# Performance work log

Measured on AMD Instinct MI355X. Metric: run time of the kernel, lower is better.

## Reference

```python
import jax, jax.numpy as jnp
import numpy as np

N, E, DIM, H, EDIM = 50000, 800000, 128, 4, 16
C = DIM // H  # per-head channels = 32

def _ln(x, g, b, eps=1e-5):
    mu = jnp.mean(x, -1, keepdims=True)
    var = jnp.mean((x - mu) ** 2, -1, keepdims=True)
    return (x - mu) * jax.lax.rsqrt(var + eps) * g + b

def setup_inputs() -> dict:
    key = jax.random.key(0)
    ks = jax.random.split(key, 16)
    s = lambda d: 1.0 / np.sqrt(d)
    inp = {
        'x': jax.random.normal(ks[0], (N, DIM), jnp.float32),
        'edge_index_s': jax.random.randint(ks[1], (2, E), 0, N, jnp.int64),
        'edge_attr_s': jax.random.normal(ks[2], (E, EDIM), jnp.float32),
        'Wq': jax.random.normal(ks[3], (DIM, DIM), jnp.float32) * s(DIM),
        'bq': jnp.zeros((DIM,), jnp.float32),
        'Wk': jax.random.normal(ks[4], (DIM, DIM), jnp.float32) * s(DIM),
        'bk': jnp.zeros((DIM,), jnp.float32),
        'Wv': jax.random.normal(ks[5], (DIM, DIM), jnp.float32) * s(DIM),
        'bv': jnp.zeros((DIM,), jnp.float32),
        'We': jax.random.normal(ks[6], (EDIM, DIM), jnp.float32) * s(EDIM),
        'be': jnp.zeros((DIM,), jnp.float32),
        'Ws': jax.random.normal(ks[7], (DIM, DIM), jnp.float32) * s(DIM),
        'bs': jnp.zeros((DIM,), jnp.float32),
        'Wbeta': jax.random.normal(ks[8], (3 * DIM, 1), jnp.float32) * s(3 * DIM),
        'g1': jnp.ones((DIM,), jnp.float32),
        'b1': jnp.zeros((DIM,), jnp.float32),
        'Wf1': jax.random.normal(ks[9], (DIM, 4 * DIM), jnp.float32) * s(DIM),
        'bf1': jnp.zeros((4 * DIM,), jnp.float32),
        'Wf2': jax.random.normal(ks[10], (4 * DIM, DIM), jnp.float32) * s(4 * DIM),
        'bf2': jnp.zeros((DIM,), jnp.float32),
        'g2': jnp.ones((DIM,), jnp.float32),
        'b2': jnp.zeros((DIM,), jnp.float32),
    }
    return inp

def reference(x, edge_index_s, edge_attr_s, Wq, bq, Wk, bk, Wv, bv, We, be,
              Ws, bs, Wbeta, g1, b1, Wf1, bf1, Wf2, bf2, g2, b2):
    src, dst = edge_index_s[0], edge_index_s[1]
    # project + reshape to [N, H, C]
    q = (x @ Wq + bq).reshape(N, H, C)
    k = (x @ Wk + bk).reshape(N, H, C)
    v = (x @ Wv + bv).reshape(N, H, C)
    e = (edge_attr_s @ We + be).reshape(E, H, C)
    # gather along edges (irregular access)
    kj = k[src] + e  # [E, H, C]
    vj = v[src] + e
    alpha = jnp.einsum('ehc,ehc->eh', q[dst], kj) / jnp.sqrt(jnp.float32(C))
    # segment softmax over incoming edges of each dst node
    m = jax.ops.segment_max(alpha, dst, num_segments=N)  # [N, H]
    a = jnp.exp(alpha - m[dst])
    denom = jax.ops.segment_sum(a, dst, num_segments=N)
    a = a / (denom[dst] + 1e-16)
    out = jax.ops.segment_sum(a[:, :, None] * vj, dst, num_segments=N)  # [N, H, C]
    out = out.reshape(N, DIM)
    # beta-gated skip (TransformerConv beta=True)
    xr = x @ Ws + bs
    beta = jax.nn.sigmoid(jnp.concatenate([out, xr, out - xr], -1) @ Wbeta)  # [N, 1]
    xs = beta * xr + (1.0 - beta) * out
    # residual + LN + FFN + LN
    h = _ln(x + xs, g1, b1)
    ff = jax.nn.relu(h @ Wf1 + bf1) @ Wf2 + bf2
    return _ln(h + ff, g2, b2)
```

## Files before the change

kernel.cpp:

```cpp
#include <hip/hip_runtime.h>
#include <hip/hip_bf16.h>

#define NN 50000
#define EE 800000
#define DIMM 128

typedef __attribute__((ext_vector_type(8))) short bf16x8;
typedef __attribute__((ext_vector_type(8))) unsigned short us8;
typedef __attribute__((ext_vector_type(4))) float f32x4;

static __device__ __forceinline__ unsigned short f2bf(float f) {
    unsigned int u = __float_as_uint(f);
    unsigned int r = (u + 0x7fffu + ((u >> 16) & 1u)) >> 16;
    return (unsigned short)r;
}
static __device__ __forceinline__ float bf2f(unsigned short s) {
    return __uint_as_float(((unsigned int)s) << 16);
}

__global__ __launch_bounds__(256) void pack_w(
    const float* __restrict__ Wq, const float* __restrict__ Wk,
    const float* __restrict__ Wv, const float* __restrict__ Ws,
    const float* __restrict__ bq, const float* __restrict__ bk,
    const float* __restrict__ bv, const float* __restrict__ bs,
    const float* __restrict__ Wf1, const float* __restrict__ Wf2,
    unsigned short* __restrict__ wqkvsT, unsigned short* __restrict__ wf1T,
    unsigned short* __restrict__ wf2T, float* __restrict__ biasq)
{
    int i = blockIdx.x * 256 + threadIdx.x;
    if (i < 65536) {
        int n = i >> 7, k = i & 127;
        int sel = n >> 7, col = n & 127;
        const float* W = sel == 0 ? Wq : sel == 1 ? Wk : sel == 2 ? Wv : Ws;
        wqkvsT[i] = f2bf(W[k * 128 + col]);
    } else if (i < 131072) {
        int j = i - 65536; int n = j >> 7, k = j & 127;
        wf1T[j] = f2bf(Wf1[k * 512 + n]);
    } else if (i < 196608) {
        int j = i - 131072; int n = j >> 9, k = j & 511;
        wf2T[j] = f2bf(Wf2[k * 128 + n]);
    } else if (i < 197120) {
        int j = i - 196608; int sel = j >> 7;
        const float* bp = sel == 0 ? bq : sel == 1 ? bk : sel == 2 ? bv : bs;
        biasq[j] = bp[j & 127];
    }
}

template<bool A_BF16, int EPI>
__global__ __launch_bounds__(256) void gemm_k(
    const void* __restrict__ Ap, const unsigned short* __restrict__ Bt,
    const float* __restrict__ bias, void* __restrict__ Cp,
    float* __restrict__ qb, unsigned short* __restrict__ kvb, float* __restrict__ xrb,
    int M, int Nn, int K)
{
    __shared__ unsigned short As[128][72];
    __shared__ unsigned short Bs[64][72];
    int tid = threadIdx.x;
    int nb = Nn >> 6;
    int bm = blockIdx.x / nb, bn = blockIdx.x % nb;
    int w = tid >> 6, lane = tid & 63;
    int wm = w >> 1, wn = w & 1;
    int lr = lane & 15, quad = lane >> 4;

    f32x4 acc[4][2];
    #pragma unroll
    for (int i = 0; i < 4; i++)
        #pragma unroll
        for (int j = 0; j < 2; j++) { f32x4 z = {0.f, 0.f, 0.f, 0.f}; acc[i][j] = z; }

    for (int kc = 0; kc < K; kc += 64) {
        #pragma unroll
        for (int it = 0; it < 4; ++it) {
            int row = it * 32 + (tid >> 3);
            int k8 = (tid & 7) * 8;
            int rg = bm * 128 + row;
            us8 st = {0, 0, 0, 0, 0, 0, 0, 0};
            if (rg < M) {
                if constexpr (A_BF16) {
                    st = *(const us8*)((const unsigned short*)Ap + (size_t)rg * K + kc + k8);
                } else {
                    const float* src = (const float*)Ap + (size_t)rg * K + kc + k8;
                    float4 f0 = *(const float4*)src;
                    float4 f1 = *(const float4*)(src + 4);
                    st[0] = f2bf(f0.x); st[1] = f2bf(f0.y); st[2] = f2bf(f0.z); st[3] = f2bf(f0.w);
                    st[4] = f2bf(f1.x); st[5] = f2bf(f1.y); st[6] = f2bf(f1.z); st[7] = f2bf(f1.w);
                }
            }
            *(us8*)&As[row][k8] = st;
        }
        {
            int nrow = tid >> 2;
            int k16 = (tid & 3) * 16;
            const unsigned short* src = Bt + (size_t)(bn * 64 + nrow) * K + kc + k16;
            *(us8*)&Bs[nrow][k16]     = *(const us8*)src;
            *(us8*)&Bs[nrow][k16 + 8] = *(const us8*)(src + 8);
        }
        __syncthreads();
        #pragma unroll
        for (int kk = 0; kk < 2; ++kk) {
            bf16x8 af[4], bfr[2];
            #pragma unroll
            for (int mi = 0; mi < 4; mi++)
                af[mi] = *(const bf16x8*)&As[wm * 64 + mi * 16 + lr][kk * 32 + quad * 8];
            #pragma unroll
            for (int ni = 0; ni < 2; ni++)
                bfr[ni] = *(const bf16x8*)&Bs[wn * 32 + ni * 16 + lr][kk * 32 + quad * 8];
            #pragma unroll
            for (int mi = 0; mi < 4; mi++)
                #pragma unroll
                for (int ni = 0; ni < 2; ni++)
                    acc[mi][ni] = __builtin_amdgcn_mfma_f32_16x16x32_bf16(af[mi], bfr[ni], acc[mi][ni], 0, 0, 0);
        }
        __syncthreads();
    }
    #pragma unroll
    for (int mi = 0; mi < 4; mi++) {
        #pragma unroll
        for (int ni = 0; ni < 2; ni++) {
            int cg = bn * 64 + wn * 32 + ni * 16 + lr;
            float bv = bias[cg];
            #pragma unroll
            for (int r = 0; r < 4; r++) {
                int rg = bm * 128 + wm * 64 + mi * 16 + quad * 4 + r;
                if (rg < M) {
                    float val = acc[mi][ni][r] + bv;
                    if constexpr (EPI == 0) {
                        ((float*)Cp)[(size_t)rg * Nn + cg] = val;
                    } else if constexpr (EPI == 1) {
                        val = fmaxf(val, 0.f);
                        ((unsigned short*)Cp)[(size_t)rg * Nn + cg] = f2bf(val);
                    } else {
                        int sel = cg >> 7, c = cg & 127;
                        if (sel == 0)      qb[(size_t)rg * 128 + c] = val;
                        else if (sel == 1) kvb[(size_t)rg * 256 + 2 * c] = f2bf(val);
                        else if (sel == 2) kvb[(size_t)rg * 256 + 2 * c + 1] = f2bf(val);
                        else               xrb[(size_t)rg * 128 + c] = val;
                    }
                }
            }
        }
    }
}

__global__ __launch_bounds__(256) void hist_k(const int* __restrict__ dst, int* __restrict__ deg) {
    int e = blockIdx.x * 256 + threadIdx.x;
    if (e < EE) atomicAdd(&deg[dst[e]], 1);
}

__global__ __launch_bounds__(256) void scan_phaseA(const int* __restrict__ deg, int* __restrict__ rs,
                                                   int* __restrict__ bsum) {
    __shared__ int sm[256];
    int tid = threadIdx.x;
    int i = blockIdx.x * 256 + tid;
    int v = (i < NN) ? deg[i] : 0;
    sm[tid] = v;
    __syncthreads();
    #pragma unroll
    for (int off = 1; off < 256; off <<= 1) {
        int t = 0;
        if (tid >= off) t = sm[tid - off];
        __syncthreads();
        if (tid >= off) sm[tid] += t;
        __syncthreads();
    }
    if (i < NN) rs[i] = sm[tid] - v;
    if (tid == 255) bsum[blockIdx.x] = sm[255];
}

__global__ __launch_bounds__(256) void scan_phaseB(int* __restrict__ bsum, int nb) {
    __shared__ int sm[256];
    int tid = threadIdx.x;
    int v = (tid < nb) ? bsum[tid] : 0;
    sm[tid] = v;
    __syncthreads();
    #pragma unroll
    for (int off = 1; off < 256; off <<= 1) {
        int t = 0;
        if (tid >= off) t = sm[tid - off];
        __syncthreads();
        if (tid >= off) sm[tid] += t;
        __syncthreads();
    }
    if (tid < nb) bsum[tid] = sm[tid] - v;
}

__global__ __launch_bounds__(256) void scan_phaseC(int* __restrict__ rs, const int* __restrict__ bsum) {
    int i = blockIdx.x * 256 + threadIdx.x;
    if (i < NN) rs[i] += bsum[blockIdx.x];
    if (i == 0) rs[NN] = EE;
}

__global__ __launch_bounds__(256) void scatter_k(
    const int* __restrict__ src, const int* __restrict__ dst,
    const float* __restrict__ eattr, const int* __restrict__ rs,
    int* __restrict__ cur, int* __restrict__ srcs_sorted,
    unsigned short* __restrict__ eas)
{
    int e = blockIdx.x * 256 + threadIdx.x;
    if (e < EE) {
        int d = dst[e];
        int p = atomicAdd(&cur[d], 1);
        int pos = rs[d] + p;
        srcs_sorted[pos] = src[e];
        const float* ap = eattr + (size_t)e * 16;
        float4 a0 = *(const float4*)ap;
        float4 a1 = *(const float4*)(ap + 4);
        float4 a2 = *(const float4*)(ap + 8);
        float4 a3 = *(const float4*)(ap + 12);
        us8 lo, hi;
        lo[0] = f2bf(a0.x); lo[1] = f2bf(a0.y); lo[2] = f2bf(a0.z); lo[3] = f2bf(a0.w);
        lo[4] = f2bf(a1.x); lo[5] = f2bf(a1.y); lo[6] = f2bf(a1.z); lo[7] = f2bf(a1.w);
        hi[0] = f2bf(a2.x); hi[1] = f2bf(a2.y); hi[2] = f2bf(a2.z); hi[3] = f2bf(a2.w);
        hi[4] = f2bf(a3.x); hi[5] = f2bf(a3.y); hi[6] = f2bf(a3.z); hi[7] = f2bf(a3.w);
        *(us8*)(eas + (size_t)pos * 16)     = lo;
        *(us8*)(eas + (size_t)pos * 16 + 8) = hi;
    }
}

__global__ __launch_bounds__(256, 3) void attn_kernel(
    const float* __restrict__ q, const unsigned int* __restrict__ kvb,
    const float* __restrict__ xr, const float* __restrict__ x,
    const unsigned short* __restrict__ eas, const int* __restrict__ srcs,
    const int* __restrict__ rs,
    const float* __restrict__ We, const float* __restrict__ be,
    const float* __restrict__ Wbeta,
    const float* __restrict__ gamma1, const float* __restrict__ beta1,
    float* __restrict__ hout, unsigned int* __restrict__ hbf)
{
    int wave = threadIdx.x >> 6;
    int lane = threadIdx.x & 63;
    int n = blockIdx.x * 4 + wave;
    if (n >= NN) return;
    int c0 = lane * 2, c1 = c0 + 1;
    int jlane = lane & 15;
    int hbase = lane & 48;

    float we0[16], we1[16];
    #pragma unroll
    for (int j = 0; j < 16; j++) { we0[j] = We[j * 128 + c0]; we1[j] = We[j * 128 + c1]; }
    float be0 = be[c0], be1 = be[c1];

    float2 q2 = *(const float2*)(q + (size_t)n * 128 + c0);
    q2.x *= 0.17677669529663687f;
    q2.y *= 0.17677669529663687f;

    float qbe = q2.x * be0 + q2.y * be1;
    qbe += __shfl_xor(qbe, 1); qbe += __shfl_xor(qbe, 2);
    qbe += __shfl_xor(qbe, 4); qbe += __shfl_xor(qbe, 8);
    float qwe = 0.f;
    #pragma unroll
    for (int j = 0; j < 16; j++) {
        float u = q2.x * we0[j] + q2.y * we1[j];
        u += __shfl_xor(u, 1); u += __shfl_xor(u, 2);
        u += __shfl_xor(u, 4); u += __shfl_xor(u, 8);
        if (jlane == j) qwe = u;
    }

    float l = 0.f, a0 = 0.f, a1 = 0.f, s = 0.f;
    int beg = rs[n], end = rs[n + 1];

    int sr_c[8]; unsigned short e_c[8];
    #pragma unroll
    for (int j = 0; j < 8; j++) {
        int idx = min(beg + j, EE - 1);
        sr_c[j] = srcs[idx];
        e_c[j] = eas[(size_t)idx * 16 + jlane];
    }
    for (int g = beg; g < end; g += 8) {
        uint2 kvp[8];
        #pragma unroll
        for (int j = 0; j < 8; j++)
            kvp[j] = *(const uint2*)(kvb + (size_t)sr_c[j] * 128 + (lane << 1));
        int gn = g + 8;
        int sr_n[8]; unsigned short e_n[8];
        #pragma unroll
        for (int j = 0; j < 8; j++) {
            int idx = min(gn + j, EE - 1);
            sr_n[j] = srcs[idx];
            e_n[j] = eas[(size_t)idx * 16 + jlane];
        }
        int cnt = end - g;
        #pragma unroll
        for (int j = 0; j < 8; j++) {
            if (j < cnt) {
                float ea = bf2f(e_c[j]);
                unsigned int kx = kvp[j].x, ky = kvp[j].y;
                float k0 = __uint_as_float(kx << 16);
                float v0 = __uint_as_float(kx & 0xffff0000u);
                float k1 = __uint_as_float(ky << 16);
                float v1 = __uint_as_float(ky & 0xffff0000u);
                float part = fmaf(q2.x, k0, fmaf(q2.y, k1, qwe * ea));
                part += __shfl_xor(part, 1);
                part += __shfl_xor(part, 2);
                part += __shfl_xor(part, 4);
                part += __shfl_xor(part, 8);
                float wgt = __expf(part + qbe);
                l += wgt;
                a0 = fmaf(wgt, v0, a0);
                a1 = fmaf(wgt, v1, a1);
                s = fmaf(wgt, ea, s);
            }
        }
        #pragma unroll
        for (int j = 0; j < 8; j++) { sr_c[j] = sr_n[j]; e_c[j] = e_n[j]; }
    }

    float eo0 = l * be0, eo1 = l * be1;
    #pragma unroll
    for (int j = 0; j < 16; j++) {
        float sj = __shfl(s, hbase + j);
        eo0 = fmaf(sj, we0[j], eo0);
        eo1 = fmaf(sj, we1[j], eo1);
    }
    a0 += eo0; a1 += eo1;

    float inv = l > 0.f ? 1.f / l : 0.f;
    float o0 = a0 * inv, o1 = a1 * inv;

    float wbo0 = Wbeta[c0],        wbo1 = Wbeta[c1];
    float wbx0 = Wbeta[128 + c0],  wbx1 = Wbeta[128 + c1];
    float wbd0 = Wbeta[256 + c0],  wbd1 = Wbeta[256 + c1];
    float2 xr2 = *(const float2*)(xr + (size_t)n * 128 + c0);
    float bl = o0 * wbo0 + o1 * wbo1 + xr2.x * wbx0 + xr2.y * wbx1
             + (o0 - xr2.x) * wbd0 + (o1 - xr2.y) * wbd1;
    #pragma unroll
    for (int off = 1; off < 64; off <<= 1) bl += __shfl_xor(bl, off);
    float beta = 1.f / (1.f + __expf(-bl));
    float xs0 = beta * xr2.x + (1.f - beta) * o0;
    float xs1 = beta * xr2.y + (1.f - beta) * o1;

    float2 xv = *(const float2*)(x + (size_t)n * 128 + c0);
    float t0 = xv.x + xs0, t1 = xv.y + xs1;
    float sm = t0 + t1;
    #pragma unroll
    for (int off = 1; off < 64; off <<= 1) sm += __shfl_xor(sm, off);
    float mu = sm * (1.f / 128.f);
    float d0 = t0 - mu, d1 = t1 - mu;
    float vv = d0 * d0 + d1 * d1;
    #pragma unroll
    for (int off = 1; off < 64; off <<= 1) vv += __shfl_xor(vv, off);
    float is = rsqrtf(vv * (1.f / 128.f) + 1e-5f);
    float h0 = d0 * is * gamma1[c0] + beta1[c0];
    float h1 = d1 * is * gamma1[c1] + beta1[c1];
    *(float2*)(hout + (size_t)n * 128 + c0) = make_float2(h0, h1);
    hbf[(size_t)n * 64 + lane] = (unsigned int)f2bf(h0) | ((unsigned int)f2bf(h1) << 16);
}

__global__ __launch_bounds__(256) void ln2_k(
    const float* __restrict__ h, const float* __restrict__ ff2,
    const float* __restrict__ gamma2, const float* __restrict__ beta2,
    float* __restrict__ out)
{
    int wave = threadIdx.x >> 6;
    int lane = threadIdx.x & 63;
    int n = blockIdx.x * 4 + wave;
    if (n >= NN) return;
    int c0 = lane * 2;
    float2 hv = *(const float2*)(h + (size_t)n * 128 + c0);
    float2 fv = *(const float2*)(ff2 + (size_t)n * 128 + c0);
    float t0 = hv.x + fv.x, t1 = hv.y + fv.y;
    float sm = t0 + t1;
    #pragma unroll
    for (int off = 1; off < 64; off <<= 1) sm += __shfl_xor(sm, off);
    float mu = sm * (1.f / 128.f);
    float d0 = t0 - mu, d1 = t1 - mu;
    float vv = d0 * d0 + d1 * d1;
    #pragma unroll
    for (int off = 1; off < 64; off <<= 1) vv += __shfl_xor(vv, off);
    float is = rsqrtf(vv * (1.f / 128.f) + 1e-5f);
    float o0 = d0 * is * gamma2[c0] + beta2[c0];
    float o1 = d1 * is * gamma2[c0 + 1] + beta2[c0 + 1];
    *(float2*)(out + (size_t)n * 128 + c0) = make_float2(o0, o1);
}

extern "C" void kernel_launch(void* const* d_in, const int* in_sizes, int n_in,
                              void* d_out, int out_size, void* d_ws, size_t ws_size,
                              hipStream_t stream) {
    const float* x      = (const float*)d_in[0];
    const int*   eindex = (const int*)d_in[1];
    const float* eattr  = (const float*)d_in[2];
    const float* Wq = (const float*)d_in[3];  const float* bq = (const float*)d_in[4];
    const float* Wk = (const float*)d_in[5];  const float* bk = (const float*)d_in[6];
    const float* Wv = (const float*)d_in[7];  const float* bv = (const float*)d_in[8];
    const float* We = (const float*)d_in[9];  const float* be = (const float*)d_in[10];
    const float* Ws = (const float*)d_in[11]; const float* bs = (const float*)d_in[12];
    const float* Wbeta = (const float*)d_in[13];
    const float* g1 = (const float*)d_in[14]; const float* b1 = (const float*)d_in[15];
    const float* Wf1 = (const float*)d_in[16]; const float* bf1 = (const float*)d_in[17];
    const float* Wf2 = (const float*)d_in[18]; const float* bf2 = (const float*)d_in[19];
    const float* g2 = (const float*)d_in[20]; const float* b2 = (const float*)d_in[21];

    char* ws = (char*)d_ws;
    size_t off = 0;
    #define ALLOC(ptr, type, bytes) type* ptr = (type*)(ws + off); off = (off + (size_t)(bytes) + 255) & ~(size_t)255;
    ALLOC(wqkvsT, unsigned short, 512 * 128 * 2)
    ALLOC(wf1T,   unsigned short, 512 * 128 * 2)
    ALLOC(wf2T,   unsigned short, 128 * 512 * 2)
    ALLOC(biasq,  float,          512 * 4)
    ALLOC(qb,     float,          (size_t)NN * 128 * 4)
    ALLOC(kvb,    unsigned short, (size_t)NN * 256 * 2)
    ALLOC(xrb,    float,          (size_t)NN * 128 * 4)
    ALLOC(h,      float,          (size_t)NN * 128 * 4)
    ALLOC(hbf,    unsigned int,   (size_t)NN * 128 * 2)
    ALLOC(deg,    int,            2 * NN * 4)
    ALLOC(row_start, int,         (NN + 1) * 4)
    ALLOC(bsum,   int,            1024)
    ALLOC(srcs_sorted, int,       (size_t)EE * 4)
    ALLOC(eas,    unsigned short, (size_t)EE * 16 * 2)
    #undef ALLOC
    int* cursor = deg + NN;
    unsigned short* ff1 = (unsigned short*)qb;
    float* ff2 = xrb;

    hipMemsetAsync(deg, 0, (size_t)2 * NN * 4, stream);

    pack_w<<<770, 256, 0, stream>>>(Wq, Wk, Wv, Ws, bq, bk, bv, bs, Wf1, Wf2,
                                    wqkvsT, wf1T, wf2T, biasq);

    gemm_k<false, 2><<<391 * 8, 256, 0, stream>>>(x, wqkvsT, biasq, nullptr,
                                                  qb, kvb, xrb, NN, 512, 128);

    hist_k<<<3125, 256, 0, stream>>>(eindex + EE, deg);
    scan_phaseA<<<196, 256, 0, stream>>>(deg, row_start, bsum);
    scan_phaseB<<<1, 256, 0, stream>>>(bsum, 196);
    scan_phaseC<<<196, 256, 0, stream>>>(row_start, bsum);
    scatter_k<<<3125, 256, 0, stream>>>(eindex, eindex + EE, eattr, row_start,
                                        cursor, srcs_sorted, eas);

    attn_kernel<<<12500, 256, 0, stream>>>(qb, (const unsigned int*)kvb, xrb, x,
                                           eas, srcs_sorted, row_start,
                                           We, be, Wbeta, g1, b1, h, hbf);

    gemm_k<true, 1><<<391 * 8, 256, 0, stream>>>(hbf, wf1T, bf1, ff1,
                                                 nullptr, nullptr, nullptr, NN, 512, 128);
    gemm_k<true, 0><<<391 * 2, 256, 0, stream>>>(ff1, wf2T, bf2, ff2,
                                                 nullptr, nullptr, nullptr, NN, 128, 512);

    ln2_k<<<12500, 256, 0, stream>>>(h, ff2, g2, b2, (float*)d_out);
}
```

Before: 527.0 us.

## Widen GEMM tiles to 128x128 and double-buffer edge gathers in attention

The GEMM kernel now computes 128x128 output tiles, with each wave owning 64x64 (4x4 MFMA accumulators). This halves B-tile reloads per output and cuts the grid size, at the cost of more registers and fewer blocks. The attention kernel drops the per-lane We register arrays and reads We directly, freeing registers. It also software-pipelines the edge loop with two alternating 8-edge buffers, so the kv gather for the next group is issued before the current group is computed, exposing more memory-level parallelism.

```diff
diff --git a/kernel.cpp b/kernel.cpp
--- a/kernel.cpp
+++ b/kernel.cpp
@@ -54,19 +54,19 @@
     int M, int Nn, int K)
 {
     __shared__ unsigned short As[128][72];
-    __shared__ unsigned short Bs[64][72];
+    __shared__ unsigned short Bs[128][72];
     int tid = threadIdx.x;
-    int nb = Nn >> 6;
+    int nb = Nn >> 7;
     int bm = blockIdx.x / nb, bn = blockIdx.x % nb;
     int w = tid >> 6, lane = tid & 63;
     int wm = w >> 1, wn = w & 1;
     int lr = lane & 15, quad = lane >> 4;
 
-    f32x4 acc[4][2];
+    f32x4 acc[4][4];
     #pragma unroll
     for (int i = 0; i < 4; i++)
         #pragma unroll
-        for (int j = 0; j < 2; j++) { f32x4 z = {0.f, 0.f, 0.f, 0.f}; acc[i][j] = z; }
+        for (int j = 0; j < 4; j++) { f32x4 z = {0.f, 0.f, 0.f, 0.f}; acc[i][j] = z; }
 
     for (int kc = 0; kc < K; kc += 64) {
         #pragma unroll
@@ -87,28 +87,22 @@
                 }
             }
             *(us8*)&As[row][k8] = st;
-        }
-        {
-            int nrow = tid >> 2;
-            int k16 = (tid & 3) * 16;
-            const unsigned short* src = Bt + (size_t)(bn * 64 + nrow) * K + kc + k16;
-            *(us8*)&Bs[nrow][k16]     = *(const us8*)src;
-            *(us8*)&Bs[nrow][k16 + 8] = *(const us8*)(src + 8);
+            *(us8*)&Bs[row][k8] = *(const us8*)(Bt + (size_t)(bn * 128 + row) * K + kc + k8);
         }
         __syncthreads();
         #pragma unroll
         for (int kk = 0; kk < 2; ++kk) {
-            bf16x8 af[4], bfr[2];
+            bf16x8 af[4], bfr[4];
             #pragma unroll
             for (int mi = 0; mi < 4; mi++)
                 af[mi] = *(const bf16x8*)&As[wm * 64 + mi * 16 + lr][kk * 32 + quad * 8];
             #pragma unroll
-            for (int ni = 0; ni < 2; ni++)
-                bfr[ni] = *(const bf16x8*)&Bs[wn * 32 + ni * 16 + lr][kk * 32 + quad * 8];
+            for (int ni = 0; ni < 4; ni++)
+                bfr[ni] = *(const bf16x8*)&Bs[wn * 64 + ni * 16 + lr][kk * 32 + quad * 8];
             #pragma unroll
             for (int mi = 0; mi < 4; mi++)
                 #pragma unroll
-                for (int ni = 0; ni < 2; ni++)
+                for (int ni = 0; ni < 4; ni++)
                     acc[mi][ni] = __builtin_amdgcn_mfma_f32_16x16x32_bf16(af[mi], bfr[ni], acc[mi][ni], 0, 0, 0);
         }
         __syncthreads();
@@ -116,8 +110,8 @@
     #pragma unroll
     for (int mi = 0; mi < 4; mi++) {
         #pragma unroll
-        for (int ni = 0; ni < 2; ni++) {
-            int cg = bn * 64 + wn * 32 + ni * 16 + lr;
+        for (int ni = 0; ni < 4; ni++) {
+            int cg = bn * 128 + wn * 64 + ni * 16 + lr;
             float bv = bias[cg];
             #pragma unroll
             for (int r = 0; r < 4; r++) {
@@ -235,9 +229,6 @@
     int jlane = lane & 15;
     int hbase = lane & 48;
 
-    float we0[16], we1[16];
-    #pragma unroll
-    for (int j = 0; j < 16; j++) { we0[j] = We[j * 128 + c0]; we1[j] = We[j * 128 + c1]; }
     float be0 = be[c0], be1 = be[c1];
 
     float2 q2 = *(const float2*)(q + (size_t)n * 128 + c0);
@@ -250,7 +241,7 @@
     float qwe = 0.f;
     #pragma unroll
     for (int j = 0; j < 16; j++) {
-        float u = q2.x * we0[j] + q2.y * we1[j];
+        float u = q2.x * We[j * 128 + c0] + q2.y * We[j * 128 + c1];
         u += __shfl_xor(u, 1); u += __shfl_xor(u, 2);
         u += __shfl_xor(u, 4); u += __shfl_xor(u, 8);
         if (jlane == j) qwe = u;
@@ -259,58 +250,65 @@
     float l = 0.f, a0 = 0.f, a1 = 0.f, s = 0.f;
     int beg = rs[n], end = rs[n + 1];
 
-    int sr_c[8]; unsigned short e_c[8];
-    #pragma unroll
-    for (int j = 0; j < 8; j++) {
-        int idx = min(beg + j, EE - 1);
-        sr_c[j] = srcs[idx];
-        e_c[j] = eas[(size_t)idx * 16 + jlane];
-    }
-    for (int g = beg; g < end; g += 8) {
-        uint2 kvp[8];
-        #pragma unroll
-        for (int j = 0; j < 8; j++)
-            kvp[j] = *(const uint2*)(kvb + (size_t)sr_c[j] * 128 + (lane << 1));
-        int gn = g + 8;
-        int sr_n[8]; unsigned short e_n[8];
-        #pragma unroll
-        for (int j = 0; j < 8; j++) {
-            int idx = min(gn + j, EE - 1);
-            sr_n[j] = srcs[idx];
-            e_n[j] = eas[(size_t)idx * 16 + jlane];
-        }
-        int cnt = end - g;
-        #pragma unroll
-        for (int j = 0; j < 8; j++) {
-            if (j < cnt) {
-                float ea = bf2f(e_c[j]);
-                unsigned int kx = kvp[j].x, ky = kvp[j].y;
-                float k0 = __uint_as_float(kx << 16);
-                float v0 = __uint_as_float(kx & 0xffff0000u);
-                float k1 = __uint_as_float(ky << 16);
-                float v1 = __uint_as_float(ky & 0xffff0000u);
-                float part = fmaf(q2.x, k0, fmaf(q2.y, k1, qwe * ea));
-                part += __shfl_xor(part, 1);
-                part += __shfl_xor(part, 2);
-                part += __shfl_xor(part, 4);
-                part += __shfl_xor(part, 8);
-                float wgt = __expf(part + qbe);
-                l += wgt;
-                a0 = fmaf(wgt, v0, a0);
-                a1 = fmaf(wgt, v1, a1);
-                s = fmaf(wgt, ea, s);
-            }
-        }
-        #pragma unroll
-        for (int j = 0; j < 8; j++) { sr_c[j] = sr_n[j]; e_c[j] = e_n[j]; }
-    }
+    int sr0[8], sr1[8];
+    unsigned short ea0[8], ea1[8];
+    uint2 kv0[8], kv1[8];
+
+#define LOADMETA(g, SR, EA) { \
+    _Pragma("unroll") \
+    for (int j = 0; j < 8; j++) { \
+        int idx = min((g) + j, EE - 1); \
+        SR[j] = srcs[idx]; \
+        EA[j] = eas[(size_t)idx * 16 + jlane]; \
+    } }
+#define GATHER(SR, KV) { \
+    _Pragma("unroll") \
+    for (int j = 0; j < 8; j++) \
+        KV[j] = *(const uint2*)(kvb + (size_t)SR[j] * 128 + (lane << 1)); }
+#define COMPUTE(g, EA, KV) { \
+    int cnt = end - (g); \
+    _Pragma("unroll") \
+    for (int j = 0; j < 8; j++) { \
+        if (j < cnt) { \
+            float ea = bf2f(EA[j]); \
+            unsigned int kx = KV[j].x, ky = KV[j].y; \
+            float k0 = __uint_as_float(kx << 16); \
+            float v0 = __uint_as_float(kx & 0xffff0000u); \
+            float k1 = __uint_as_float(ky << 16); \
+            float v1 = __uint_as_float(ky & 0xffff0000u); \
+            float part = fmaf(q2.x, k0, fmaf(q2.y, k1, qwe * ea)); \
+            part += __shfl_xor(part, 1); \
+            part += __shfl_xor(part, 2); \
+            part += __shfl_xor(part, 4); \
+            part += __shfl_xor(part, 8); \
+            float wgt = __expf(part + qbe); \
+            l += wgt; \
+            a0 = fmaf(wgt, v0, a0); \
+            a1 = fmaf(wgt, v1, a1); \
+            s = fmaf(wgt, ea, s); \
+        } } }
+
+    LOADMETA(beg, sr0, ea0)
+    GATHER(sr0, kv0)
+    LOADMETA(beg + 8, sr1, ea1)
+    for (int g = beg; g < end; g += 16) {
+        GATHER(sr1, kv1)
+        COMPUTE(g, ea0, kv0)
+        LOADMETA(g + 16, sr0, ea0)
+        GATHER(sr0, kv0)
+        COMPUTE(g + 8, ea1, kv1)
+        LOADMETA(g + 24, sr1, ea1)
+    }
+#undef LOADMETA
+#undef GATHER
+#undef COMPUTE
 
     float eo0 = l * be0, eo1 = l * be1;
     #pragma unroll
     for (int j = 0; j < 16; j++) {
         float sj = __shfl(s, hbase + j);
-        eo0 = fmaf(sj, we0[j], eo0);
-        eo1 = fmaf(sj, we1[j], eo1);
+        eo0 = fmaf(sj, We[j * 128 + c0], eo0);
+        eo1 = fmaf(sj, We[j * 128 + c1], eo1);
     }
     a0 += eo0; a1 += eo1;
 
@@ -417,7 +415,7 @@
     pack_w<<<770, 256, 0, stream>>>(Wq, Wk, Wv, Ws, bq, bk, bv, bs, Wf1, Wf2,
                                     wqkvsT, wf1T, wf2T, biasq);
 
-    gemm_k<false, 2><<<391 * 8, 256, 0, stream>>>(x, wqkvsT, biasq, nullptr,
+    gemm_k<false, 2><<<391 * 4, 256, 0, stream>>>(x, wqkvsT, biasq, nullptr,
                                                   qb, kvb, xrb, NN, 512, 128);
 
     hist_k<<<3125, 256, 0, stream>>>(eindex + EE, deg);
@@ -431,9 +429,9 @@
                                            eas, srcs_sorted, row_start,
                                            We, be, Wbeta, g1, b1, h, hbf);
 
-    gemm_k<true, 1><<<391 * 8, 256, 0, stream>>>(hbf, wf1T, bf1, ff1,
+    gemm_k<true, 1><<<391 * 4, 256, 0, stream>>>(hbf, wf1T, bf1, ff1,
                                                  nullptr, nullptr, nullptr, NN, 512, 128);
-    gemm_k<true, 0><<<391 * 2, 256, 0, stream>>>(ff1, wf2T, bf2, ff2,
+    gemm_k<true, 0><<<391 * 1, 256, 0, stream>>>(ff1, wf2T, bf2, ff2,
                                                  nullptr, nullptr, nullptr, NN, 128, 512);
 
     ln2_k<<<12500, 256, 0, stream>>>(h, ff2, g2, b2, (float*)d_out);
```

Result: no change. 531.7 us (+0.9%).
